# Kernel tuning notes

Hardware: AMD Instinct MI355X
Metric: run time of the kernel (lower is better)

The kernel has to match this reference:

```python
import jax, jax.numpy as jnp
import numpy as np

OUT_FEATURES = 11008
IN_FEATURES = 4096
GROUP_SIZE = 32
NUM_GROUPS = OUT_FEATURES * IN_FEATURES // GROUP_SIZE        # 1,409,024
NUM_PACKED = NUM_GROUPS * (GROUP_SIZE // 8 * 3)              # 16,908,288 bytes


def block_dequantize_3bit(weight_q3, weight_norm):
    """Unpack 3-bit codes (8 values per 3 bytes) and dequantize to fp32."""
    p = weight_q3.reshape(-1, 3).astype(jnp.int32)  # [N/8, 3] bytes
    b0, b1, b2 = p[:, 0], p[:, 1], p[:, 2]
    q = jnp.stack([
        b0 & 7,
        (b0 >> 3) & 7,
        ((b0 >> 6) & 3) | ((b1 & 1) << 2),
        (b1 >> 1) & 7,
        (b1 >> 4) & 7,
        ((b1 >> 7) & 1) | ((b2 & 3) << 1),
        (b2 >> 2) & 7,
        (b2 >> 5) & 7,
    ], axis=-1)                                     # [N/8, 8] codes in 0..7
    q = q.reshape(NUM_GROUPS, GROUP_SIZE).astype(jnp.float32)
    norm = weight_norm.astype(jnp.float32)[:, None]  # [num_groups, 1]
    w = (q / 7.0) * 2.0 * norm - norm                # map [0,7] -> [-norm, norm]
    return w.reshape(OUT_FEATURES, IN_FEATURES)


def setup_inputs() -> dict:
    key = jax.random.key(0)
    k1, k2, k3, k4 = jax.random.split(key, 4)
    x = jax.random.normal(k1, (4, 128, IN_FEATURES), dtype=jnp.float32)
    weight_q3 = jax.random.randint(k2, (NUM_PACKED,), 0, 256, dtype=jnp.int32)
    weight_norm = (jax.random.uniform(k3, (NUM_GROUPS,), dtype=jnp.float32) * 0.1 + 0.01).astype(jnp.float16)
    bias = jax.random.normal(k4, (OUT_FEATURES,), dtype=jnp.float32) * 0.02
    return {"x": x, "weight_q3": weight_q3, "weight_norm": weight_norm, "bias": bias}


def reference(x, weight_q3, weight_norm, bias):
    w = block_dequantize_3bit(weight_q3, weight_norm)  # [out, in] fp32
    return jnp.einsum('bsd,od->bso', x, w) + bias
```

## Files before the change

kernel.cpp:

```cpp
#include <hip/hip_runtime.h>
#include <hip/hip_fp16.h>

#define M_TOTAL 512
#define N_TOTAL 11008
#define K_TOTAL 4096
#define BM 128
#define BN 64
#define BK 64
#define NT (K_TOTAL / BK)
#define NUM_GROUPS (N_TOTAL * K_TOTAL / 32)
#define LDK 72

typedef short bf16x8 __attribute__((ext_vector_type(8)));
typedef _Float16 fp16x8 __attribute__((ext_vector_type(8)));
typedef float f32x4 __attribute__((ext_vector_type(4)));

__device__ __forceinline__ unsigned int pack2_bf16(float f0, float f1) {
    unsigned int u0 = __builtin_bit_cast(unsigned int, f0) + 0x8000u;
    unsigned int u1 = __builtin_bit_cast(unsigned int, f1) + 0x8000u;
    return (u0 >> 16) | (u1 & 0xFFFF0000u);
}

__device__ __forceinline__ void async_ld16(void* lds, const void* g) {
    __builtin_amdgcn_global_load_lds(
        (const __attribute__((address_space(1))) unsigned int*)g,
        (__attribute__((address_space(3))) unsigned int*)lds, 16, 0, 0);
}

__device__ __forceinline__ int detect_mode_wave(const void* __restrict__ wn) {
    const int lane = threadIdx.x & 63;
    const unsigned short* u16 = (const unsigned short*)wn;
    const float* f32p = (const float*)wn;
    const float vb = __builtin_bit_cast(float, (unsigned int)u16[lane] << 16);
    const float vh = __half2float(__builtin_bit_cast(__half, u16[lane]));
    const float vf = f32p[lane];
    const unsigned long long mb = __ballot(vb > 0.005f && vb < 0.12f);
    const unsigned long long mh = __ballot(vh > 0.005f && vh < 0.12f);
    (void)vf;
    return (mb == ~0ull) ? 2 : ((mh == ~0ull) ? 1 : 0);
}

__device__ __forceinline__ float load_norm_mode(const void* __restrict__ wn,
                                                int mode, int g) {
    if (mode == 0)      return ((const float*)wn)[g];
    else if (mode == 1) return __half2float(((const __half*)wn)[g]);
    else                return __builtin_bit_cast(float,
                           (unsigned int)((const unsigned short*)wn)[g] << 16);
}

__global__ void __launch_bounds__(256)
convert_x_kernel(const float* __restrict__ x, unsigned short* __restrict__ xb) {
    const int i = (blockIdx.x * 256 + threadIdx.x) * 4;
    const float4 v = *(const float4*)&x[i];
    const __half2 p0 = __floats2half2_rn(v.x, v.y);
    const __half2 p1 = __floats2half2_rn(v.z, v.w);
    *(uint2*)&xb[i] = make_uint2(__builtin_bit_cast(unsigned int, p0),
                                 __builtin_bit_cast(unsigned int, p1));
}

__global__ void __launch_bounds__(256)
decode_w_kernel(const int* __restrict__ wq, const void* __restrict__ wnorm,
                unsigned short* __restrict__ wf) {
    const int mode = detect_mode_wave(wnorm);
    const int g = blockIdx.x * 256 + threadIdx.x;
    const int4* wq4 = (const int4*)wq;
    const int4 w0 = wq4[g * 3];
    const int4 w1 = wq4[g * 3 + 1];
    const int4 w2 = wq4[g * 3 + 2];
    const float nrm = load_norm_mode(wnorm, mode, g);
    const __half2 A2 = __float2half2_rn(nrm * (16.0f / 7.0f));
    const __half2 B2 = __float2half2_rn(nrm * (-23.0f / 7.0f));
    const unsigned int bits_s[4] = {
        (unsigned)w0.x | ((unsigned)w0.y << 8) | ((unsigned)w0.z << 16),
        (unsigned)w0.w | ((unsigned)w1.x << 8) | ((unsigned)w1.y << 16),
        (unsigned)w1.z | ((unsigned)w1.w << 8) | ((unsigned)w2.x << 16),
        (unsigned)w2.y | ((unsigned)w2.z << 8) | ((unsigned)w2.w << 16)};
    unsigned int packs[16];
#pragma unroll
    for (int s = 0; s < 4; ++s) {
        const unsigned int bits = bits_s[s];
#pragma unroll
        for (int j = 0; j < 4; ++j) {
            const unsigned int q0 = (bits >> (6 * j)) & 7u;
            const unsigned int q1 = (bits >> (6 * j + 3)) & 7u;
            const unsigned int y  = 0x3C003C00u | (q0 << 7) | (q1 << 23);
            packs[s * 4 + j] = __builtin_bit_cast(unsigned int,
                __hfma2(__builtin_bit_cast(__half2, y), A2, B2));
        }
    }
    const int o  = g >> 7;
    const int kb = (g & 127) * 32;
    uint4* dst = (uint4*)&wf[(size_t)o * K_TOTAL + kb];
    dst[0] = make_uint4(packs[0], packs[1], packs[2], packs[3]);
    dst[1] = make_uint4(packs[4], packs[5], packs[6], packs[7]);
    dst[2] = make_uint4(packs[8], packs[9], packs[10], packs[11]);
    dst[3] = make_uint4(packs[12], packs[13], packs[14], packs[15]);
}

__global__ void __launch_bounds__(256, 3)
l3b_gemm_ws(const unsigned short* __restrict__ xb, const unsigned short* __restrict__ wf,
            const float* __restrict__ bias, float* __restrict__ out)
{
    __shared__ unsigned short As[2][BM * 64];
    __shared__ unsigned short Bs[2][BN * 64];

    const int tid = threadIdx.x;

    const int bid = blockIdx.x;
    const int w   = (bid & 7) * 86 + (bid >> 3);
    const int m0  = (w & 3) * BM;
    const int n0  = (w >> 2) * BN;

    const int wid  = tid >> 6;
    const int lane = tid & 63;
    const int quad = lane >> 4;
    const int lm   = lane & 15;
    const int wm   = (wid >> 1) * 64;
    const int wn_  = (wid & 1) * 32;

    const int row0  = wid * 8 + (lane >> 3);
    const int gcol  = ((lane & 7) ^ ((lane >> 3) & 7)) * 8;
    const int slot  = (lane & 7) * 8;

    auto stageA = [&](int it, int buf) {
#pragma unroll
        for (int j = 0; j < 4; ++j) {
            const int row = row0 + j * 32;
            async_ld16(&As[buf][(row << 6) + slot],
                       &xb[(size_t)(m0 + row) * K_TOTAL + it * 64 + gcol]);
        }
    };
    auto stageB = [&](int it, int buf) {
#pragma unroll
        for (int j = 0; j < 2; ++j) {
            const int row = row0 + j * 32;
            async_ld16(&Bs[buf][(row << 6) + slot],
                       &wf[(size_t)(n0 + row) * K_TOTAL + it * 64 + gcol]);
        }
    };

    f32x4 acc[4][2];
#pragma unroll
    for (int i = 0; i < 4; ++i)
#pragma unroll
        for (int j = 0; j < 2; ++j) acc[i][j] = (f32x4){0.f, 0.f, 0.f, 0.f};

    auto mfmaTile = [&](const unsigned short* Asb, const unsigned short* Bsb) {
#pragma unroll
        for (int ks = 0; ks < 2; ++ks) {
            const int cswz = (((ks * 4 + quad) ^ (lm & 7)) << 3);
            fp16x8 aF[4], bF[2];
#pragma unroll
            for (int mi = 0; mi < 4; ++mi)
                aF[mi] = *(const fp16x8*)&Asb[((wm + mi * 16 + lm) << 6) + cswz];
#pragma unroll
            for (int ni = 0; ni < 2; ++ni)
                bF[ni] = *(const fp16x8*)&Bsb[((wn_ + ni * 16 + lm) << 6) + cswz];
            __builtin_amdgcn_s_setprio(1);
#pragma unroll
            for (int mi = 0; mi < 4; ++mi)
#pragma unroll
                for (int ni = 0; ni < 2; ++ni)
                    acc[mi][ni] = __builtin_amdgcn_mfma_f32_16x16x32_f16(
                        aF[mi], bF[ni], acc[mi][ni], 0, 0, 0);
            __builtin_amdgcn_s_setprio(0);
        }
    };

    stageA(0, 0);
    stageB(0, 0);
    __syncthreads();

    for (int it = 0; it < NT; ++it) {
        const int buf = it & 1;
        if (it + 1 < NT) { stageA(it + 1, buf ^ 1); stageB(it + 1, buf ^ 1); }
        mfmaTile(As[buf], Bs[buf]);
        __syncthreads();
    }

#pragma unroll
    for (int ni = 0; ni < 2; ++ni) {
        const int o  = n0 + wn_ + ni * 16 + lm;
        const float bv = bias[o];
#pragma unroll
        for (int mi = 0; mi < 4; ++mi) {
#pragma unroll
            for (int r = 0; r < 4; ++r) {
                const int m = m0 + wm + mi * 16 + quad * 4 + r;
                out[m * N_TOTAL + o] = acc[mi][ni][r] + bv;
            }
        }
    }
}

__global__ void __launch_bounds__(256, 3)
l3b_gemm_pipe(const unsigned short* __restrict__ xb, const int* __restrict__ wq,
              const void* __restrict__ wnorm, const float* __restrict__ bias,
              float* __restrict__ out)
{
    __shared__ unsigned short As[2][BM * 64];

    const int tid  = threadIdx.x;
    const int mode = detect_mode_wave(wnorm);

    const int bid = blockIdx.x;
    const int w   = (bid & 7) * 86 + (bid >> 3);
    const int m0  = (w & 3) * BM;
    const int n0  = (w >> 2) * BN;

    const int wid  = tid >> 6;
    const int lane = tid & 63;
    const int quad = lane >> 4;
    const int lm   = lane & 15;
    const int wm   = (wid >> 1) * 64;
    const int wn_  = (wid & 1) * 32;

    const int arow0 = wid * 8 + (lane >> 3);
    const int acol  = ((lane & 7) ^ ((lane >> 3) & 7)) * 8;
    const int aslot = (lane & 7) * 8;

    auto stageA = [&](int it, int buf) {
#pragma unroll
        for (int j = 0; j < 4; ++j) {
            const int row = arow0 + j * 32;
            async_ld16(&As[buf][(row << 6) + aslot],
                       &xb[(size_t)(m0 + row) * K_TOTAL + it * 64 + acol]);
        }
    };

    struct BP { int b0[4], b1[4], b2[4]; float nrm[4]; };

    auto loadBP = [&](int it, BP& P) {
#pragma unroll
        for (int u = 0; u < 4; ++u) {
            const int ks = u >> 1, ni = u & 1;
            const int c  = n0 + wn_ + ni * 16 + lm;
            const int g  = c * (K_TOTAL / 32) + it * 2 + ks;
            const int base = g * 12 + quad * 3;
            P.b0[u] = ((const int*)wq)[base];
            P.b1[u] = ((const int*)wq)[base + 1];
            P.b2[u] = ((const int*)wq)[base + 2];
            P.nrm[u] = load_norm_mode(wnorm, mode, g);
        }
    };

    auto decodeBF = [&](int b0, int b1, int b2, float nrm) -> fp16x8 {
        const __half2 A2 = __float2half2_rn(nrm * (16.0f / 7.0f));
        const __half2 B2 = __float2half2_rn(nrm * (-23.0f / 7.0f));
        const unsigned int bits =
            (unsigned)b0 | ((unsigned)b1 << 8) | ((unsigned)b2 << 16);
        union { unsigned int u[4]; fp16x8 v; } r;
#pragma unroll
        for (int j = 0; j < 4; ++j) {
            const unsigned int q0 = (bits >> (6 * j)) & 7u;
            const unsigned int q1 = (bits >> (6 * j + 3)) & 7u;
            const unsigned int y  = 0x3C003C00u | (q0 << 7) | (q1 << 23);
            r.u[j] = __builtin_bit_cast(unsigned int,
                       __hfma2(__builtin_bit_cast(__half2, y), A2, B2));
        }
        return r.v;
    };

    f32x4 acc[4][2];
#pragma unroll
    for (int i = 0; i < 4; ++i)
#pragma unroll
        for (int j = 0; j < 2; ++j) acc[i][j] = (f32x4){0.f, 0.f, 0.f, 0.f};

    auto mfmaStep = [&](const unsigned short* Asb, const BP& P) {
#pragma unroll
        for (int ks = 0; ks < 2; ++ks) {
            const int cswz = (((ks * 4 + quad) ^ (lm & 7)) << 3);
            fp16x8 aF[4];
#pragma unroll
            for (int mi = 0; mi < 4; ++mi)
                aF[mi] = *(const fp16x8*)&Asb[((wm + mi * 16 + lm) << 6) + cswz];
#pragma unroll
            for (int ni = 0; ni < 2; ++ni) {
                const int u = ks * 2 + ni;
                const fp16x8 bF = decodeBF(P.b0[u], P.b1[u], P.b2[u], P.nrm[u]);
                __builtin_amdgcn_s_setprio(1);
#pragma unroll
                for (int mi = 0; mi < 4; ++mi)
                    acc[mi][ni] = __builtin_amdgcn_mfma_f32_16x16x32_f16(
                        aF[mi], bF, acc[mi][ni], 0, 0, 0);
                __builtin_amdgcn_s_setprio(0);
            }
        }
    };

    BP Pa, Pb;

    stageA(0, 0);
    loadBP(0, Pa);
    __syncthreads();

    for (int it = 0; it < NT; it += 2) {
        stageA(it + 1, 1);
        __builtin_amdgcn_sched_barrier(0);
        loadBP(it + 1, Pb);
        __builtin_amdgcn_sched_barrier(0);
        mfmaStep(As[0], Pa);
        __builtin_amdgcn_sched_barrier(0);
        if (it + 2 < NT) {
            asm volatile("s_waitcnt vmcnt(16)" ::: "memory");
        } else {
            asm volatile("s_waitcnt vmcnt(0)" ::: "memory");
        }
        __builtin_amdgcn_s_barrier();
        __builtin_amdgcn_sched_barrier(0);

        if (it + 2 < NT) stageA(it + 2, 0);
        __builtin_amdgcn_sched_barrier(0);
        if (it + 2 < NT) loadBP(it + 2, Pa);
        __builtin_amdgcn_sched_barrier(0);
        mfmaStep(As[1], Pb);
        __builtin_amdgcn_sched_barrier(0);
        if (it + 2 < NT) {
            asm volatile("s_waitcnt vmcnt(16)" ::: "memory");
        } else {
            asm volatile("s_waitcnt vmcnt(0)" ::: "memory");
        }
        __builtin_amdgcn_s_barrier();
        __builtin_amdgcn_sched_barrier(0);
    }

#pragma unroll
    for (int ni = 0; ni < 2; ++ni) {
        const int o  = n0 + wn_ + ni * 16 + lm;
        const float bv = bias[o];
#pragma unroll
        for (int mi = 0; mi < 4; ++mi) {
#pragma unroll
            for (int r = 0; r < 4; ++r) {
                const int m = m0 + wm + mi * 16 + quad * 4 + r;
                out[m * N_TOTAL + o] = acc[mi][ni][r] + bv;
            }
        }
    }
}

__global__ void __launch_bounds__(256)
l3b_gemm_kernel(const float* __restrict__ x, const int* __restrict__ wq,
                const void* __restrict__ wnorm, const float* __restrict__ bias,
                float* __restrict__ out)
{
    __shared__ unsigned short As[128 * LDK];
    __shared__ unsigned short Bs[64 * LDK];

    const int mode = detect_mode_wave(wnorm);
    const int tid  = threadIdx.x;
    const int m0   = blockIdx.y * 128;
    const int n0   = blockIdx.x * 64;
    const int wid  = tid >> 6;
    const int lane = tid & 63;
    const int quad = lane >> 4;
    const int lm   = lane & 15;
    const int wm   = (wid >> 1) * 64;
    const int wn   = (wid & 1) * 32;

    f32x4 acc[4][2];
#pragma unroll
    for (int i = 0; i < 4; ++i)
#pragma unroll
        for (int j = 0; j < 2; ++j) acc[i][j] = (f32x4){0.f, 0.f, 0.f, 0.f};

    const int ar = tid >> 4;
    const int ac = (tid & 15) * 4;
    const int gin      = tid >> 1;
    const int half     = tid & 1;
    const int bn_local = gin >> 1;
    const int bkg      = gin & 1;

    for (int it = 0; it < NT; ++it) {
        const int k0 = it * BK;
        __syncthreads();
#pragma unroll
        for (int p = 0; p < 8; ++p) {
            const int row = p * 16 + ar;
            const float4 v = *(const float4*)&x[(m0 + row) * K_TOTAL + k0 + ac];
            *(uint2*)&As[row * LDK + ac] =
                make_uint2(pack2_bf16(v.x, v.y), pack2_bf16(v.z, v.w));
        }
        {
            const int g    = (n0 + bn_local) * (K_TOTAL / 32) + it * 2 + bkg;
            const int base = g * 12 + half * 6;
            const int2 w0 = *(const int2*)&wq[base];
            const int2 w1 = *(const int2*)&wq[base + 2];
            const int2 w2 = *(const int2*)&wq[base + 4];
            float nrm = load_norm_mode(wnorm, mode, g);
            const float a = nrm * (2.0f / 7.0f);
            const float b = -nrm;
            const unsigned int bits0 =
                (unsigned)w0.x | ((unsigned)w0.y << 8) | ((unsigned)w1.x << 16);
            const unsigned int bits1 =
                (unsigned)w1.y | ((unsigned)w2.x << 8) | ((unsigned)w2.y << 16);
            unsigned int packs[8];
#pragma unroll
            for (int t3 = 0; t3 < 2; ++t3) {
                const unsigned int bits = t3 ? bits1 : bits0;
#pragma unroll
                for (int j = 0; j < 4; ++j) {
                    const float f0 = fmaf((float)((bits >> (6 * j)) & 7), a, b);
                    const float f1 = fmaf((float)((bits >> (6 * j + 3)) & 7), a, b);
                    packs[t3 * 4 + j] = pack2_bf16(f0, f1);
                }
            }
            unsigned int* dst = (unsigned int*)&Bs[bn_local * LDK + bkg * 32 + half * 16];
            *(uint4*)dst       = make_uint4(packs[0], packs[1], packs[2], packs[3]);
            *(uint4*)(dst + 4) = make_uint4(packs[4], packs[5], packs[6], packs[7]);
        }
        __syncthreads();
#pragma unroll
        for (int ks = 0; ks < 2; ++ks) {
            const int kb = ks * 32 + quad * 8;
            bf16x8 aF[4], bF[2];
#pragma unroll
            for (int mi = 0; mi < 4; ++mi)
                aF[mi] = *(const bf16x8*)&As[(wm + mi * 16 + lm) * LDK + kb];
#pragma unroll
            for (int ni = 0; ni < 2; ++ni)
                bF[ni] = *(const bf16x8*)&Bs[(wn + ni * 16 + lm) * LDK + kb];
#pragma unroll
            for (int mi = 0; mi < 4; ++mi)
#pragma unroll
                for (int ni = 0; ni < 2; ++ni)
                    acc[mi][ni] = __builtin_amdgcn_mfma_f32_16x16x32_bf16(
                        aF[mi], bF[ni], acc[mi][ni], 0, 0, 0);
        }
    }
#pragma unroll
    for (int ni = 0; ni < 2; ++ni) {
        const int o  = n0 + wn + ni * 16 + lm;
        const float bv = bias[o];
#pragma unroll
        for (int mi = 0; mi < 4; ++mi)
#pragma unroll
            for (int r = 0; r < 4; ++r) {
                const int m = m0 + wm + mi * 16 + quad * 4 + r;
                out[m * N_TOTAL + o] = acc[mi][ni][r] + bv;
            }
    }
}

extern "C" void kernel_launch(void* const* d_in, const int* in_sizes, int n_in,
                              void* d_out, int out_size, void* d_ws, size_t ws_size,
                              hipStream_t stream) {
    const float* x    = (const float*)d_in[0];
    const int*   wq   = (const int*)d_in[1];
    const void*  wn   = d_in[2];
    const float* bias = (const float*)d_in[3];
    float* out = (float*)d_out;

    const size_t xbBytes = (size_t)M_TOTAL * K_TOTAL * 2;
    const size_t wfBytes = (size_t)N_TOTAL * K_TOTAL * 2;
    const size_t need_full = 256 + xbBytes + wfBytes;
    const size_t need_mid  = 256 + xbBytes;

    if (ws_size >= need_full) {
        unsigned short* xb = (unsigned short*)((char*)d_ws + 256);
        unsigned short* wf = (unsigned short*)((char*)d_ws + 256 + xbBytes);
        convert_x_kernel<<<(M_TOTAL * K_TOTAL / 4) / 256, 256, 0, stream>>>(x, xb);
        decode_w_kernel<<<NUM_GROUPS / 256, 256, 0, stream>>>(wq, wn, wf);
        l3b_gemm_ws<<<(M_TOTAL / BM) * (N_TOTAL / BN), 256, 0, stream>>>(
            xb, wf, bias, out);
    } else if (ws_size >= need_mid) {
        unsigned short* xb = (unsigned short*)((char*)d_ws + 256);
        convert_x_kernel<<<(M_TOTAL * K_TOTAL / 4) / 256, 256, 0, stream>>>(x, xb);
        l3b_gemm_pipe<<<(M_TOTAL / BM) * (N_TOTAL / BN), 256, 0, stream>>>(
            xb, wq, wn, bias, out);
    } else {
        dim3 grid(N_TOTAL / 64, M_TOTAL / 128);
        l3b_gemm_kernel<<<grid, 256, 0, stream>>>(x, wq, wn, bias, out);
    }
}
```

Baseline: 195.1 us.

## Split-K GEMM in two halves with atomics and direct-to-register B loads

Splits the K dimension of the workspace GEMM into two halves, doubling the grid to 1376 blocks and combining the partial sums with atomicAdd into an output zeroed by a memset. The B tile no longer goes through LDS; each lane loads its MFMA fragments straight from global memory into registers, double-buffered across two register sets, and occupancy is raised to 4 blocks per CU. This targets the tail and occupancy cost of only 688 tiles on a large GPU. In exchange it adds a full output memset, atomic write traffic, and uncoalesced global B loads.

```diff
diff --git a/kernel.cpp b/kernel.cpp
--- a/kernel.cpp
+++ b/kernel.cpp
@@ -8,6 +8,7 @@
 #define BN 64
 #define BK 64
 #define NT (K_TOTAL / BK)
+#define NT_HALF 32
 #define NUM_GROUPS (N_TOTAL * K_TOTAL / 32)
 #define LDK 72
 
@@ -97,19 +98,22 @@
     dst[3] = make_uint4(packs[12], packs[13], packs[14], packs[15]);
 }
 
-__global__ void __launch_bounds__(256, 3)
+__global__ void __launch_bounds__(256, 4)
 l3b_gemm_ws(const unsigned short* __restrict__ xb, const unsigned short* __restrict__ wf,
             const float* __restrict__ bias, float* __restrict__ out)
 {
     __shared__ unsigned short As[2][BM * 64];
-    __shared__ unsigned short Bs[2][BN * 64];
 
     const int tid = threadIdx.x;
 
-    const int bid = blockIdx.x;
-    const int w   = (bid & 7) * 86 + (bid >> 3);
-    const int m0  = (w & 3) * BM;
-    const int n0  = (w >> 2) * BN;
+    const int bid   = blockIdx.x;
+    const int w     = (bid & 7) * 172 + (bid >> 3);
+    const int khalf = w / 688;
+    const int tile  = w - khalf * 688;
+    const int m0    = (tile & 3) * BM;
+    const int n0    = (tile >> 2) * BN;
+    const int it0   = khalf * NT_HALF;
+    const int itEnd = it0 + NT_HALF;
 
     const int wid  = tid >> 6;
     const int lane = tid & 63;
@@ -118,25 +122,29 @@
     const int wm   = (wid >> 1) * 64;
     const int wn_  = (wid & 1) * 32;
 
-    const int row0  = wid * 8 + (lane >> 3);
-    const int gcol  = ((lane & 7) ^ ((lane >> 3) & 7)) * 8;
-    const int slot  = (lane & 7) * 8;
+    const int arow0 = wid * 8 + (lane >> 3);
+    const int acol  = ((lane & 7) ^ ((lane >> 3) & 7)) * 8;
+    const int aslot = (lane & 7) * 8;
 
     auto stageA = [&](int it, int buf) {
 #pragma unroll
         for (int j = 0; j < 4; ++j) {
-            const int row = row0 + j * 32;
-            async_ld16(&As[buf][(row << 6) + slot],
-                       &xb[(size_t)(m0 + row) * K_TOTAL + it * 64 + gcol]);
-        }
-    };
-    auto stageB = [&](int it, int buf) {
-#pragma unroll
-        for (int j = 0; j < 2; ++j) {
-            const int row = row0 + j * 32;
-            async_ld16(&Bs[buf][(row << 6) + slot],
-                       &wf[(size_t)(n0 + row) * K_TOTAL + it * 64 + gcol]);
-        }
+            const int row = arow0 + j * 32;
+            async_ld16(&As[buf][(row << 6) + aslot],
+                       &xb[(size_t)(m0 + row) * K_TOTAL + it * 64 + acol]);
+        }
+    };
+
+    const size_t cBase0 = (size_t)(n0 + wn_ + lm) * K_TOTAL + quad * 8;
+    const size_t cBase1 = (size_t)(n0 + wn_ + 16 + lm) * K_TOTAL + quad * 8;
+
+    struct BF { fp16x8 f[4]; };
+    auto loadB = [&](int it, BF& F) {
+        const int k0 = it * 64;
+        F.f[0] = *(const fp16x8*)&wf[cBase0 + k0];
+        F.f[1] = *(const fp16x8*)&wf[cBase1 + k0];
+        F.f[2] = *(const fp16x8*)&wf[cBase0 + k0 + 32];
+        F.f[3] = *(const fp16x8*)&wf[cBase1 + k0 + 32];
     };
 
     f32x4 acc[4][2];
@@ -145,49 +153,52 @@
 #pragma unroll
         for (int j = 0; j < 2; ++j) acc[i][j] = (f32x4){0.f, 0.f, 0.f, 0.f};
 
-    auto mfmaTile = [&](const unsigned short* Asb, const unsigned short* Bsb) {
+    auto mfmaTile = [&](const unsigned short* Asb, const BF& F) {
 #pragma unroll
         for (int ks = 0; ks < 2; ++ks) {
             const int cswz = (((ks * 4 + quad) ^ (lm & 7)) << 3);
-            fp16x8 aF[4], bF[2];
+            fp16x8 aF[4];
 #pragma unroll
             for (int mi = 0; mi < 4; ++mi)
                 aF[mi] = *(const fp16x8*)&Asb[((wm + mi * 16 + lm) << 6) + cswz];
-#pragma unroll
-            for (int ni = 0; ni < 2; ++ni)
-                bF[ni] = *(const fp16x8*)&Bsb[((wn_ + ni * 16 + lm) << 6) + cswz];
             __builtin_amdgcn_s_setprio(1);
 #pragma unroll
             for (int mi = 0; mi < 4; ++mi)
 #pragma unroll
                 for (int ni = 0; ni < 2; ++ni)
                     acc[mi][ni] = __builtin_amdgcn_mfma_f32_16x16x32_f16(
-                        aF[mi], bF[ni], acc[mi][ni], 0, 0, 0);
+                        aF[mi], F.f[ks * 2 + ni], acc[mi][ni], 0, 0, 0);
             __builtin_amdgcn_s_setprio(0);
         }
     };
 
-    stageA(0, 0);
-    stageB(0, 0);
+    BF Pa, Pb;
+
+    stageA(it0, 0);
+    loadB(it0, Pa);
     __syncthreads();
 
-    for (int it = 0; it < NT; ++it) {
-        const int buf = it & 1;
-        if (it + 1 < NT) { stageA(it + 1, buf ^ 1); stageB(it + 1, buf ^ 1); }
-        mfmaTile(As[buf], Bs[buf]);
+    for (int it = it0; it < itEnd; it += 2) {
+        stageA(it + 1, 1);
+        if (it + 1 < itEnd) loadB(it + 1, Pb);
+        mfmaTile(As[0], Pa);
+        __syncthreads();
+
+        if (it + 2 < itEnd) { stageA(it + 2, 0); loadB(it + 2, Pa); }
+        mfmaTile(As[1], Pb);
         __syncthreads();
     }
 
 #pragma unroll
     for (int ni = 0; ni < 2; ++ni) {
         const int o  = n0 + wn_ + ni * 16 + lm;
-        const float bv = bias[o];
+        const float bv = (khalf == 0) ? bias[o] : 0.0f;
 #pragma unroll
         for (int mi = 0; mi < 4; ++mi) {
 #pragma unroll
             for (int r = 0; r < 4; ++r) {
                 const int m = m0 + wm + mi * 16 + quad * 4 + r;
-                out[m * N_TOTAL + o] = acc[mi][ni][r] + bv;
+                atomicAdd(&out[m * N_TOTAL + o], acc[mi][ni][r] + bv);
             }
         }
     }
@@ -460,9 +471,10 @@
     if (ws_size >= need_full) {
         unsigned short* xb = (unsigned short*)((char*)d_ws + 256);
         unsigned short* wf = (unsigned short*)((char*)d_ws + 256 + xbBytes);
+        hipMemsetAsync(out, 0, (size_t)M_TOTAL * N_TOTAL * sizeof(float), stream);
         convert_x_kernel<<<(M_TOTAL * K_TOTAL / 4) / 256, 256, 0, stream>>>(x, xb);
         decode_w_kernel<<<NUM_GROUPS / 256, 256, 0, stream>>>(wq, wn, wf);
-        l3b_gemm_ws<<<(M_TOTAL / BM) * (N_TOTAL / BN), 256, 0, stream>>>(
+        l3b_gemm_ws<<<(M_TOTAL / BM) * (N_TOTAL / BN) * 2, 256, 0, stream>>>(
             xb, wf, bias, out);
     } else if (ws_size >= need_mid) {
         unsigned short* xb = (unsigned short*)((char*)d_ws + 256);
```

After: 272.9 us. +39.9%, slower.
